# Performance work log

Measured on AMD Instinct MI355X. Metric: run time of the kernel, lower is better.

Reference implementation:

```python
import jax, jax.numpy as jnp
import numpy as np

B, N, K, D, L = 8, 1024, 16, 256, 3  # batch, max_node_num, neighbor fan-in, g_hidden_dim, layers


def setup_inputs() -> dict:
    key = jax.random.key(0)
    ks = jax.random.split(key, 14)
    f32 = jnp.float32
    scale = 1.0 / np.sqrt(D).astype(np.float32)
    randn = lambda k, s: jax.random.normal(k, s, dtype=f32)
    lens = jax.random.randint(ks[12], (B,), N // 2, N + 1)
    node_mask = (jnp.arange(N)[None, :] < lens[:, None]).astype(f32)
    return {
        "h0": randn(ks[0], (B, N, D)),
        "c0": randn(ks[1], (B, N, D)),
        "x_in": randn(ks[2], (B, N, D)),
        "x_out": randn(ks[3], (B, N, D)),
        "W_in": randn(ks[4], (4, D, D)) * scale,   # gates stacked: [i, o, f, cell]
        "U_in": randn(ks[5], (4, D, D)) * scale,
        "W_out": randn(ks[6], (4, D, D)) * scale,
        "U_out": randn(ks[7], (4, D, D)) * scale,
        "b": jnp.zeros((4, D), dtype=f32),
        "in_mask": jax.random.randint(ks[8], (B, N, K), 0, 2).astype(f32),
        "out_mask": jax.random.randint(ks[9], (B, N, K), 0, 2).astype(f32),
        "node_mask": node_mask,
        "in_nodes": jax.random.randint(ks[10], (B, N, K), 0, N, dtype=jnp.int32),
        "out_nodes": jax.random.randint(ks[11], (B, N, K), 0, N, dtype=jnp.int32),
        "num_layers": L,
    }


def _gather_agg(h, idx, nb_mask, node_mask):
    # h: [B,N,D], idx: [B,N,K] -> masked sum of neighbor hidden states [B,N,D]
    nb = jax.vmap(lambda hb, ib: hb[ib])(h, idx)           # [B,N,K,D]
    agg = jnp.einsum('bnkd,bnk->bnd', nb, nb_mask)
    return agg * node_mask[..., None]


def reference(h0, c0, x_in, x_out, W_in, U_in, W_out, U_out, b,
              in_mask, out_mask, node_mask, in_nodes, out_nodes, num_layers):
    h, c = h0, c0
    nm = node_mask[..., None]
    for _ in range(num_layers):
        h_in = _gather_agg(h, in_nodes, in_mask, node_mask)
        h_out = _gather_agg(h, out_nodes, out_mask, node_mask)
        # pre-activation for all 4 gates at once: [4,B,N,D]
        pre = (jnp.einsum('bnd,gde->gbne', x_in, W_in)
               + jnp.einsum('bnd,gde->gbne', h_in, U_in)
               + jnp.einsum('bnd,gde->gbne', x_out, W_out)
               + jnp.einsum('bnd,gde->gbne', h_out, U_out)
               + b[:, None, None, :])
        i_g = jax.nn.sigmoid(pre[0])
        o_g = jax.nn.sigmoid(pre[1])
        f_g = jax.nn.sigmoid(pre[2])
        g = jnp.tanh(pre[3])
        c = (f_g * c + i_g * g) * nm
        h = o_g * jnp.tanh(c) * nm
    return h
```

## Files before the change

### kernel.cpp

```cpp
#include <hip/hip_runtime.h>
#include <hip/hip_bf16.h>
#include <cstdint>
#include <cstddef>

typedef __hip_bfloat16 bf16;
typedef _Float16 f16;
typedef __attribute__((ext_vector_type(4))) float f32x4;
typedef __attribute__((ext_vector_type(8))) _Float16 f16x8;
typedef __attribute__((ext_vector_type(4))) _Float16 f16x4;
typedef __attribute__((ext_vector_type(4))) unsigned short u16x4;

#define BB 8
#define NN 1024
#define KK 16
#define DD 256
#define MM (BB * NN)
#define NLAYER 3

__device__ __forceinline__ float ldf(const void* p, size_t i, int isf32) {
  return isf32 ? ((const float*)p)[i] : __bfloat162float(((const bf16*)p)[i]);
}

__device__ __forceinline__ f32x4 ldf4(const void* p, size_t vi, int isf32) {
  f32x4 r;
  if (isf32) {
    r = ((const f32x4*)p)[vi];
  } else {
    u16x4 u = ((const u16x4*)p)[vi];
#pragma unroll
    for (int q = 0; q < 4; q++) {
      union { unsigned u; float f; } c;
      c.u = ((unsigned)u[q]) << 16;
      r[q] = c.f;
    }
  }
  return r;
}

__device__ __forceinline__ void gload_lds16(const void* g, void* l) {
  __builtin_amdgcn_global_load_lds(
      (const __attribute__((address_space(1))) unsigned int*)g,
      (__attribute__((address_space(3))) unsigned int*)l, 16, 0, 0);
}

__device__ __forceinline__ int detect_isf32_wave(const void* W) {
  int lane = threadIdx.x & 63;
  unsigned short b = ((const unsigned short*)W)[2 * lane];
  int e = (b >> 7) & 0xFF;
  int sane = ((e >= 105 && e <= 130) || (b & 0x7FFF) == 0) ? 1 : 0;
  unsigned long long m = __ballot(sane);
  return (__popcll(m) > 32) ? 0 : 1;
}

__device__ __forceinline__ float fsigmoid(float x) {
  float a = fminf(fmaxf(-1.44269504f * x, -126.f), 126.f);
  float e = __builtin_amdgcn_exp2f(a);
  return __builtin_amdgcn_rcpf(1.f + e);
}
__device__ __forceinline__ float ftanh(float x) {
  float a = fminf(fmaxf(2.88539008f * x, -126.f), 126.f);
  float e = __builtin_amdgcn_exp2f(a);
  return 1.f - 2.f * __builtin_amdgcn_rcpf(1.f + e);
}

struct Params {
  const void *h0, *c0, *x_in, *x_out, *W_in, *U_in, *W_out, *U_out, *bvec;
  const void *in_mask, *out_mask, *node_mask;
  const int *in_nodes, *out_nodes;
  float *biasI, *nmF, *inmF, *outmF, *XW;
  f16 *h_cur, *c_cur, *A_buf, *X_buf, *BT_W, *BT_U;
  void* outp;
};

#define PREP_VEC_TOTAL (256 + 2048 + 32768 + 32768 + 524288 + 524288)
#define PREP_BLOCKS (256 + (PREP_VEC_TOTAL + 255) / 256)
__global__ void prep_k(Params p) {
  __shared__ float tile[64][65];
  int isf32 = detect_isf32_wave(p.W_in);
  int b = blockIdx.x;
  int t = threadIdx.x;

  if (b < 256) {
    int bx = b & 3, by = (b >> 2) & 3, z = b >> 4;
    int g = z & 3, which = z >> 2;
    const void* src = (which == 0) ? p.W_in : (which == 1) ? p.W_out
                     : (which == 2) ? p.U_in : p.U_out;
    f16* dst = (which < 2) ? p.BT_W : p.BT_U;
    int colofs = (which & 1) * 256;
    size_t gbase = (size_t)g * DD * DD;
    int tx = t & 63, ty = t >> 6;
    int d0 = bx * 64, e0 = by * 64;
#pragma unroll
    for (int r = 0; r < 64; r += 4)
      tile[ty + r][tx] = ldf(src, gbase + (size_t)(d0 + ty + r) * DD + e0 + tx, isf32);
    __syncthreads();
#pragma unroll
    for (int r = 0; r < 64; r += 4)
      dst[(size_t)(4 * (e0 + ty + r) + g) * 512 + colofs + d0 + tx] = (f16)tile[tx][ty + r];
    return;
  }

  size_t i = (size_t)(b - 256) * 256 + t;
  const size_t V0 = 256;
  const size_t V1 = V0 + 2048;
  const size_t V2 = V1 + 32768;
  const size_t V3 = V2 + 32768;
  const size_t V4 = V3 + 524288;
  const size_t V5 = V4 + 524288;
  if (i < V0) {
    f32x4 r;
#pragma unroll
    for (int g = 0; g < 4; g++) r[g] = ldf(p.bvec, (size_t)g * 256 + i, isf32);
    ((f32x4*)p.biasI)[i] = r;
  } else if (i < V1) {
    ((f32x4*)p.nmF)[i - V0] = ldf4(p.node_mask, i - V0, isf32);
  } else if (i < V2) {
    ((f32x4*)p.inmF)[i - V1] = ldf4(p.in_mask, i - V1, isf32);
  } else if (i < V3) {
    ((f32x4*)p.outmF)[i - V2] = ldf4(p.out_mask, i - V2, isf32);
  } else if (i < V4) {
    size_t j = i - V3;
    f32x4 hv = ldf4(p.h0, j, isf32);
    f32x4 cv = ldf4(p.c0, j, isf32);
    f16x4 ho, co;
#pragma unroll
    for (int q = 0; q < 4; q++) { ho[q] = (f16)hv[q]; co[q] = (f16)cv[q]; }
    ((f16x4*)p.h_cur)[j] = ho;
    ((f16x4*)p.c_cur)[j] = co;
  } else if (i < V5) {
    size_t j = i - V4;
    size_t m = j >> 6, d4 = (j & 63) * 4;
    f32x4 xi = ldf4(p.x_in, j, isf32);
    f32x4 xo = ldf4(p.x_out, j, isf32);
    f16x4 a, bq;
#pragma unroll
    for (int q = 0; q < 4; q++) { a[q] = (f16)xi[q]; bq[q] = (f16)xo[q]; }
    *(f16x4*)(p.X_buf + m * 512 + d4)       = a;
    *(f16x4*)(p.X_buf + m * 512 + 256 + d4) = bq;
  }
}

__global__ void gather_k(Params p) {
  int wave = threadIdx.x >> 6;
  int lane = threadIdx.x & 63;
  int m = blockIdx.x * 4 + wave;
  int l5 = lane & 31, dir = lane >> 5;
  int myidx = 0; float mymask = 0.f;
  if (lane < 16)      { myidx = p.in_nodes[(size_t)m * KK + lane];
                        mymask = p.inmF[(size_t)m * KK + lane]; }
  else if (lane < 32) { myidx = p.out_nodes[(size_t)m * KK + lane - 16];
                        mymask = p.outmF[(size_t)m * KK + lane - 16]; }
  const f16* hb = p.h_cur + (size_t)(m >> 10) * NN * DD;
  float acc[8] = {};
#pragma unroll
  for (int k = 0; k < KK; k++) {
    int src = dir * 16 + k;
    int idxk = __shfl(myidx, src);
    float wk = __shfl(mymask, src);
    f16x8 v = *(const f16x8*)(hb + (size_t)idxk * DD + l5 * 8);
#pragma unroll
    for (int q = 0; q < 8; q++) acc[q] += wk * (float)v[q];
  }
  float nm = p.nmF[m];
  f16x8 o;
#pragma unroll
  for (int q = 0; q < 8; q++) o[q] = (f16)(acc[q] * nm);
  *(f16x8*)(p.A_buf + (size_t)m * 512 + dir * 256 + l5 * 8) = o;
}

__device__ __forceinline__ void gemm_core(const f16* gA, const f16* gB, char* smem,
                                          int t, int mBase, int nBase,
                                          f32x4 (&acc)[4][4]) {
  f16* As = (f16*)smem;
  f16* Bs = (f16*)(smem + 16384);
  int w = t >> 6, lane = t & 63;
  int wr = w >> 1, wc = w & 1;
  int row16 = lane & 15, kgrp = lane >> 4;
  int aoff[2][4], boff[2][4];
#pragma unroll
  for (int sub = 0; sub < 2; sub++) {
    int ch = ((sub * 4 + kgrp) ^ (row16 & 7)) * 8;
#pragma unroll
    for (int i = 0; i < 4; i++) aoff[sub][i] = (wr * 64 + 16 * i + row16) * 64 + ch;
#pragma unroll
    for (int j = 0; j < 4; j++) boff[sub][j] = (wc * 64 + 16 * j + row16) * 64 + ch;
  }
  int srow = t >> 3;
  int scol = ((t & 7) ^ (srow & 7)) * 8;
  const f16* ga0 = gA + (size_t)(mBase + srow) * 512 + scol;
  const f16* gb0 = gB + (size_t)(nBase + srow) * 512 + scol;
  for (int kt = 0; kt < 512; kt += 64) {
#pragma unroll
    for (int q = 0; q < 4; q++)
      gload_lds16(ga0 + kt + (size_t)(32 * q) * 512, As + q * 2048 + t * 8);
#pragma unroll
    for (int q = 0; q < 4; q++)
      gload_lds16(gb0 + kt + (size_t)(32 * q) * 512, Bs + q * 2048 + t * 8);
    __syncthreads();
#pragma unroll
    for (int sub = 0; sub < 2; sub++) {
      f16x8 af[4], bfr[4];
#pragma unroll
      for (int i = 0; i < 4; i++) af[i] = *(const f16x8*)(As + aoff[sub][i]);
#pragma unroll
      for (int j = 0; j < 4; j++) bfr[j] = *(const f16x8*)(Bs + boff[sub][j]);
#pragma unroll
      for (int i = 0; i < 4; i++)
#pragma unroll
        for (int j = 0; j < 4; j++)
          acc[i][j] = __builtin_amdgcn_mfma_f32_16x16x32_f16(af[i], bfr[j], acc[i][j], 0, 0, 0);
    }
    __syncthreads();
  }
}

__global__ __launch_bounds__(256, 3)
void gemmx_k(Params p) {
  __shared__ char smem[32768];
  int t = threadIdx.x;
  int w = t >> 6, lane = t & 63;
  int wc = w & 1, row16 = lane & 15;
  int mBase = blockIdx.x * 128, nBase = blockIdx.y * 128;
  f32x4 acc[4][4] = {};
  gemm_core(p.X_buf, p.BT_W, smem, t, mBase, nBase, acc);
  float bb[4];
#pragma unroll
  for (int j = 0; j < 4; j++) bb[j] = p.biasI[nBase + wc * 64 + 16 * j + row16];
  f32x4* dst = (f32x4*)p.XW + ((size_t)(blockIdx.y * 64 + blockIdx.x) * 256 + t) * 16;
#pragma unroll
  for (int i = 0; i < 4; i++)
#pragma unroll
    for (int j = 0; j < 4; j++) {
      f32x4 v = acc[i][j];
#pragma unroll
      for (int r = 0; r < 4; r++) v[r] += bb[j];
      dst[i * 4 + j] = v;
    }
}

__global__ __launch_bounds__(256, 3)
void gemm_k(Params p, int last) {
  __shared__ char smem[32768];
  float* tileF = (float*)smem;
  int isf32 = detect_isf32_wave(p.W_in);
  int t = threadIdx.x;
  int w = t >> 6, lane = t & 63;
  int wr = w >> 1, wc = w & 1;
  int row16 = lane & 15, kgrp = lane >> 4;
  int mBase = blockIdx.x * 128, nBase = blockIdx.y * 128;
  f32x4 acc[4][4];
  const f32x4* xw = (const f32x4*)p.XW + ((size_t)(blockIdx.y * 64 + blockIdx.x) * 256 + t) * 16;
#pragma unroll
  for (int i = 0; i < 4; i++)
#pragma unroll
    for (int j = 0; j < 4; j++) acc[i][j] = xw[i * 4 + j];
  gemm_core(p.A_buf, p.BT_U, smem, t, mBase, nBase, acc);

#pragma unroll
  for (int pp = 0; pp < 2; pp++) {
    __syncthreads();
    if (wc == pp) {
#pragma unroll
      for (int i = 0; i < 4; i++)
#pragma unroll
        for (int j = 0; j < 4; j++) {
          int cl = 16 * j + row16;
#pragma unroll
          for (int r = 0; r < 4; r++) {
            int rr = wr * 64 + 16 * i + 4 * kgrp + r;
            int ch = (cl >> 2) ^ (rr & 7);
            tileF[rr * 64 + ch * 4 + (cl & 3)] = acc[i][j][r];
          }
        }
    }
    __syncthreads();
    int el = t & 15;
    int nb = nBase + 64 * pp;
    int eb = nb >> 2;
#pragma unroll
    for (int rep = 0; rep < 8; rep++) {
      int ml = rep * 16 + (t >> 4);
      int gm = mBase + ml;
      f32x4 vals = *(const f32x4*)(tileF + ml * 64 + ((el ^ (ml & 7))) * 4);
      float nm = p.nmF[gm];
      size_t ci = (size_t)gm * DD + eb + el;
      float cold = (float)p.c_cur[ci];
      float ig = fsigmoid(vals[0]);
      float og = fsigmoid(vals[1]);
      float fg = fsigmoid(vals[2]);
      float gg = ftanh(vals[3]);
      float cn = (fg * cold + ig * gg) * nm;
      float hn = og * ftanh(cn) * nm;
      p.c_cur[ci] = (f16)cn;
      p.h_cur[ci] = (f16)hn;
      if (last) {
        if (isf32) ((float*)p.outp)[ci] = hn;
        else       ((bf16*)p.outp)[ci] = __float2bfloat16(hn);
      }
    }
  }
}

extern "C" void kernel_launch(void* const* d_in, const int* in_sizes, int n_in,
                              void* d_out, int out_size, void* d_ws, size_t ws_size,
                              hipStream_t stream) {
  char* ws = (char*)d_ws;
  f16*   h_cur = (f16*)(ws + 256);
  f16*   c_cur = h_cur + (size_t)MM * DD;
  f16*   A_buf = c_cur + (size_t)MM * DD;
  f16*   X_buf = A_buf + (size_t)MM * 512;
  f16*   BT_W  = X_buf + (size_t)MM * 512;
  f16*   BT_U  = BT_W + (size_t)1024 * 512;
  float* XW    = (float*)(BT_U + (size_t)1024 * 512);
  float* biasI = XW + (size_t)MM * 1024;
  float* nmF   = biasI + 1024;
  float* inmF  = nmF + MM;
  float* outmF = inmF + (size_t)MM * KK;

  Params p;
  p.h0 = d_in[0]; p.c0 = d_in[1]; p.x_in = d_in[2]; p.x_out = d_in[3];
  p.W_in = d_in[4]; p.U_in = d_in[5]; p.W_out = d_in[6]; p.U_out = d_in[7];
  p.bvec = d_in[8]; p.in_mask = d_in[9]; p.out_mask = d_in[10]; p.node_mask = d_in[11];
  p.in_nodes = (const int*)d_in[12]; p.out_nodes = (const int*)d_in[13];
  p.biasI = biasI; p.nmF = nmF; p.inmF = inmF; p.outmF = outmF; p.XW = XW;
  p.h_cur = h_cur; p.c_cur = c_cur; p.A_buf = A_buf; p.X_buf = X_buf;
  p.BT_W = BT_W; p.BT_U = BT_U;
  p.outp = d_out;

  prep_k<<<PREP_BLOCKS, 256, 0, stream>>>(p);
  gemmx_k<<<dim3(MM / 128, 8), 256, 0, stream>>>(p);
  for (int l = 0; l < NLAYER; l++) {
    gather_k<<<MM / 4, 256, 0, stream>>>(p);
    gemm_k<<<dim3(MM / 128, 8), 256, 0, stream>>>(p, l == NLAYER - 1);
  }
}
```

Baseline: 225.3 us.

## Fuse all phases into one persistent cooperative kernel with grid barriers

Replaces the eight separate launches (prep, input GEMM, and three gather/recurrent-GEMM pairs) with one persistent kernel of 512 blocks that runs each phase in turn, separated by a software grid barrier built on atomics. Gather work is redistributed so each block handles 16 nodes, and the first gather overlaps with the input GEMM inside the same barrier interval. The aim is to remove per-launch overhead and the tail gaps between kernels. In exchange it adds barrier spin costs, caps occupancy at 2 blocks per CU through the launch bound, and relies on all blocks being co-resident, with a non-cooperative fallback that could deadlock.

```diff
diff --git a/kernel.cpp b/kernel.cpp
--- a/kernel.cpp
+++ b/kernel.cpp
@@ -16,6 +16,8 @@
 #define DD 256
 #define MM (BB * NN)
 #define NLAYER 3
+#define NBLK 512
+#define NTHR 256
 
 __device__ __forceinline__ float ldf(const void* p, size_t i, int isf32) {
   return isf32 ? ((const float*)p)[i] : __bfloat162float(((const bf16*)p)[i]);
@@ -69,18 +71,33 @@
   const int *in_nodes, *out_nodes;
   float *biasI, *nmF, *inmF, *outmF, *XW;
   f16 *h_cur, *c_cur, *A_buf, *X_buf, *BT_W, *BT_U;
+  unsigned* bar;
   void* outp;
 };
 
+__device__ __forceinline__ void grid_sync(unsigned* bar) {
+  __syncthreads();
+  if (threadIdx.x == 0) {
+    __threadfence();
+    unsigned gen = atomicAdd(&bar[0], 0u);
+    if (atomicAdd(&bar[1], 1u) == (unsigned)gridDim.x - 1u) {
+      atomicExch(&bar[1], 0u);
+      atomicAdd(&bar[0], 1u);
+    } else {
+      while (atomicAdd(&bar[0], 0u) == gen) __builtin_amdgcn_s_sleep(2);
+    }
+    __threadfence();
+  }
+  __syncthreads();
+}
+
 #define PREP_VEC_TOTAL (256 + 2048 + 32768 + 32768 + 524288 + 524288)
-#define PREP_BLOCKS (256 + (PREP_VEC_TOTAL + 255) / 256)
-__global__ void prep_k(Params p) {
-  __shared__ float tile[64][65];
-  int isf32 = detect_isf32_wave(p.W_in);
+__device__ void prep_phase(const Params& p, char* smem, int isf32) {
   int b = blockIdx.x;
   int t = threadIdx.x;
 
   if (b < 256) {
+    float (*tile)[65] = (float(*)[65])smem;
     int bx = b & 3, by = (b >> 2) & 3, z = b >> 4;
     int g = z & 3, which = z >> 2;
     const void* src = (which == 0) ? p.W_in : (which == 1) ? p.W_out
@@ -97,75 +114,78 @@
 #pragma unroll
     for (int r = 0; r < 64; r += 4)
       dst[(size_t)(4 * (e0 + ty + r) + g) * 512 + colofs + d0 + tx] = (f16)tile[tx][ty + r];
-    return;
-  }
-
-  size_t i = (size_t)(b - 256) * 256 + t;
+  }
+
   const size_t V0 = 256;
   const size_t V1 = V0 + 2048;
   const size_t V2 = V1 + 32768;
   const size_t V3 = V2 + 32768;
   const size_t V4 = V3 + 524288;
   const size_t V5 = V4 + 524288;
-  if (i < V0) {
-    f32x4 r;
-#pragma unroll
-    for (int g = 0; g < 4; g++) r[g] = ldf(p.bvec, (size_t)g * 256 + i, isf32);
-    ((f32x4*)p.biasI)[i] = r;
-  } else if (i < V1) {
-    ((f32x4*)p.nmF)[i - V0] = ldf4(p.node_mask, i - V0, isf32);
-  } else if (i < V2) {
-    ((f32x4*)p.inmF)[i - V1] = ldf4(p.in_mask, i - V1, isf32);
-  } else if (i < V3) {
-    ((f32x4*)p.outmF)[i - V2] = ldf4(p.out_mask, i - V2, isf32);
-  } else if (i < V4) {
-    size_t j = i - V3;
-    f32x4 hv = ldf4(p.h0, j, isf32);
-    f32x4 cv = ldf4(p.c0, j, isf32);
-    f16x4 ho, co;
-#pragma unroll
-    for (int q = 0; q < 4; q++) { ho[q] = (f16)hv[q]; co[q] = (f16)cv[q]; }
-    ((f16x4*)p.h_cur)[j] = ho;
-    ((f16x4*)p.c_cur)[j] = co;
-  } else if (i < V5) {
-    size_t j = i - V4;
-    size_t m = j >> 6, d4 = (j & 63) * 4;
-    f32x4 xi = ldf4(p.x_in, j, isf32);
-    f32x4 xo = ldf4(p.x_out, j, isf32);
-    f16x4 a, bq;
-#pragma unroll
-    for (int q = 0; q < 4; q++) { a[q] = (f16)xi[q]; bq[q] = (f16)xo[q]; }
-    *(f16x4*)(p.X_buf + m * 512 + d4)       = a;
-    *(f16x4*)(p.X_buf + m * 512 + 256 + d4) = bq;
-  }
-}
-
-__global__ void gather_k(Params p) {
-  int wave = threadIdx.x >> 6;
-  int lane = threadIdx.x & 63;
-  int m = blockIdx.x * 4 + wave;
+  for (size_t i = (size_t)b * NTHR + t; i < V5; i += (size_t)NBLK * NTHR) {
+    if (i < V0) {
+      f32x4 r;
+#pragma unroll
+      for (int g = 0; g < 4; g++) r[g] = ldf(p.bvec, (size_t)g * 256 + i, isf32);
+      ((f32x4*)p.biasI)[i] = r;
+    } else if (i < V1) {
+      ((f32x4*)p.nmF)[i - V0] = ldf4(p.node_mask, i - V0, isf32);
+    } else if (i < V2) {
+      ((f32x4*)p.inmF)[i - V1] = ldf4(p.in_mask, i - V1, isf32);
+    } else if (i < V3) {
+      ((f32x4*)p.outmF)[i - V2] = ldf4(p.out_mask, i - V2, isf32);
+    } else if (i < V4) {
+      size_t j = i - V3;
+      f32x4 hv = ldf4(p.h0, j, isf32);
+      f32x4 cv = ldf4(p.c0, j, isf32);
+      f16x4 ho, co;
+#pragma unroll
+      for (int q = 0; q < 4; q++) { ho[q] = (f16)hv[q]; co[q] = (f16)cv[q]; }
+      ((f16x4*)p.h_cur)[j] = ho;
+      ((f16x4*)p.c_cur)[j] = co;
+    } else {
+      size_t j = i - V4;
+      size_t m = j >> 6, d4 = (j & 63) * 4;
+      f32x4 xi = ldf4(p.x_in, j, isf32);
+      f32x4 xo = ldf4(p.x_out, j, isf32);
+      f16x4 a, bq;
+#pragma unroll
+      for (int q = 0; q < 4; q++) { a[q] = (f16)xi[q]; bq[q] = (f16)xo[q]; }
+      *(f16x4*)(p.X_buf + m * 512 + d4)       = a;
+      *(f16x4*)(p.X_buf + m * 512 + 256 + d4) = bq;
+    }
+  }
+}
+
+__device__ void gather_phase(const Params& p) {
+  int gid = blockIdx.x, t = threadIdx.x;
+  int wave = t >> 6, lane = t & 63;
   int l5 = lane & 31, dir = lane >> 5;
-  int myidx = 0; float mymask = 0.f;
-  if (lane < 16)      { myidx = p.in_nodes[(size_t)m * KK + lane];
-                        mymask = p.inmF[(size_t)m * KK + lane]; }
-  else if (lane < 32) { myidx = p.out_nodes[(size_t)m * KK + lane - 16];
-                        mymask = p.outmF[(size_t)m * KK + lane - 16]; }
-  const f16* hb = p.h_cur + (size_t)(m >> 10) * NN * DD;
-  float acc[8] = {};
-#pragma unroll
-  for (int k = 0; k < KK; k++) {
-    int src = dir * 16 + k;
-    int idxk = __shfl(myidx, src);
-    float wk = __shfl(mymask, src);
-    f16x8 v = *(const f16x8*)(hb + (size_t)idxk * DD + l5 * 8);
-#pragma unroll
-    for (int q = 0; q < 8; q++) acc[q] += wk * (float)v[q];
-  }
-  float nm = p.nmF[m];
-  f16x8 o;
-#pragma unroll
-  for (int q = 0; q < 8; q++) o[q] = (f16)(acc[q] * nm);
-  *(f16x8*)(p.A_buf + (size_t)m * 512 + dir * 256 + l5 * 8) = o;
+#pragma unroll
+  for (int it = 0; it < 4; it++) {
+    int m = gid * 16 + it * 4 + wave;
+    int myidx = 0; float mymask = 0.f;
+    if (lane < 16)      { myidx = p.in_nodes[(size_t)m * KK + lane];
+                          mymask = p.inmF[(size_t)m * KK + lane]; }
+    else if (lane < 32) { myidx = p.out_nodes[(size_t)m * KK + lane - 16];
+                          mymask = p.outmF[(size_t)m * KK + lane - 16]; }
+    const f16* hb = p.h_cur + (size_t)(m >> 10) * NN * DD;
+    float acc[8] = {};
+#pragma unroll
+    for (int k = 0; k < KK; k++) {
+      int src = dir * 16 + k;
+      int idxk = __shfl(myidx, src);
+      float wk = __shfl(mymask, src);
+      f16x8 v = *(const f16x8*)(hb + (size_t)idxk * DD + l5 * 8);
+#pragma unroll
+      for (int q = 0; q < 8; q++) acc[q] += wk * (float)v[q];
+    }
+    float nm = p.nmF[m];
+    f16x8 o;
+#pragma unroll
+    for (int q = 0; q < 8; q++) o[q] = (f16)(acc[q] * nm);
+    *(f16x8*)(p.A_buf + (size_t)m * 512 + dir * 256 + l5 * 8) = o;
+  }
 }
 
 __device__ __forceinline__ void gemm_core(const f16* gA, const f16* gB, char* smem,
@@ -214,42 +234,38 @@
   }
 }
 
-__global__ __launch_bounds__(256, 3)
-void gemmx_k(Params p) {
-  __shared__ char smem[32768];
-  int t = threadIdx.x;
+__device__ void gemmx_phase(const Params& p, char* smem) {
+  int gid = blockIdx.x, t = threadIdx.x;
   int w = t >> 6, lane = t & 63;
   int wc = w & 1, row16 = lane & 15;
-  int mBase = blockIdx.x * 128, nBase = blockIdx.y * 128;
+  int mb = gid & 63, nb = gid >> 6;
   f32x4 acc[4][4] = {};
-  gemm_core(p.X_buf, p.BT_W, smem, t, mBase, nBase, acc);
-  float bb[4];
-#pragma unroll
-  for (int j = 0; j < 4; j++) bb[j] = p.biasI[nBase + wc * 64 + 16 * j + row16];
-  f32x4* dst = (f32x4*)p.XW + ((size_t)(blockIdx.y * 64 + blockIdx.x) * 256 + t) * 16;
+  gemm_core(p.X_buf, p.BT_W, smem, t, mb * 128, nb * 128, acc);
+  float bb4[4];
+#pragma unroll
+  for (int j = 0; j < 4; j++) bb4[j] = p.biasI[nb * 128 + wc * 64 + 16 * j + row16];
+  f32x4* dst = (f32x4*)p.XW + ((size_t)(nb * 64 + mb) * 256 + t) * 16;
 #pragma unroll
   for (int i = 0; i < 4; i++)
 #pragma unroll
     for (int j = 0; j < 4; j++) {
       f32x4 v = acc[i][j];
 #pragma unroll
-      for (int r = 0; r < 4; r++) v[r] += bb[j];
+      for (int r = 0; r < 4; r++) v[r] += bb4[j];
       dst[i * 4 + j] = v;
     }
 }
 
-__global__ __launch_bounds__(256, 3)
-void gemm_k(Params p, int last) {
-  __shared__ char smem[32768];
+__device__ void gemm_phase(const Params& p, char* smem, int last, int isf32) {
   float* tileF = (float*)smem;
-  int isf32 = detect_isf32_wave(p.W_in);
-  int t = threadIdx.x;
+  int gid = blockIdx.x, t = threadIdx.x;
   int w = t >> 6, lane = t & 63;
   int wr = w >> 1, wc = w & 1;
   int row16 = lane & 15, kgrp = lane >> 4;
-  int mBase = blockIdx.x * 128, nBase = blockIdx.y * 128;
+  int mb = gid & 63, nb = gid >> 6;
+  int mBase = mb * 128, nBase = nb * 128;
   f32x4 acc[4][4];
-  const f32x4* xw = (const f32x4*)p.XW + ((size_t)(blockIdx.y * 64 + blockIdx.x) * 256 + t) * 16;
+  const f32x4* xw = (const f32x4*)p.XW + ((size_t)(nb * 64 + mb) * 256 + t) * 16;
 #pragma unroll
   for (int i = 0; i < 4; i++)
 #pragma unroll
@@ -275,8 +291,8 @@
     }
     __syncthreads();
     int el = t & 15;
-    int nb = nBase + 64 * pp;
-    int eb = nb >> 2;
+    int nb2 = nBase + 64 * pp;
+    int eb = nb2 >> 2;
 #pragma unroll
     for (int rep = 0; rep < 8; rep++) {
       int ml = rep * 16 + (t >> 4);
@@ -301,6 +317,27 @@
   }
 }
 
+__global__ __launch_bounds__(NTHR, 2)
+void fused_k(Params p) {
+  __shared__ __attribute__((aligned(16))) char smem[32768];
+  int isf32 = detect_isf32_wave(p.W_in);
+
+  prep_phase(p, smem, isf32);
+  grid_sync(p.bar);
+  gather_phase(p);
+  gemmx_phase(p, smem);
+  grid_sync(p.bar);
+  gemm_phase(p, smem, 0, isf32);
+  grid_sync(p.bar);
+  gather_phase(p);
+  grid_sync(p.bar);
+  gemm_phase(p, smem, 0, isf32);
+  grid_sync(p.bar);
+  gather_phase(p);
+  grid_sync(p.bar);
+  gemm_phase(p, smem, 1, isf32);
+}
+
 extern "C" void kernel_launch(void* const* d_in, const int* in_sizes, int n_in,
                               void* d_out, int out_size, void* d_ws, size_t ws_size,
                               hipStream_t stream) {
@@ -325,12 +362,13 @@
   p.biasI = biasI; p.nmF = nmF; p.inmF = inmF; p.outmF = outmF; p.XW = XW;
   p.h_cur = h_cur; p.c_cur = c_cur; p.A_buf = A_buf; p.X_buf = X_buf;
   p.BT_W = BT_W; p.BT_U = BT_U;
+  p.bar = (unsigned*)ws;
   p.outp = d_out;
 
-  prep_k<<<PREP_BLOCKS, 256, 0, stream>>>(p);
-  gemmx_k<<<dim3(MM / 128, 8), 256, 0, stream>>>(p);
-  for (int l = 0; l < NLAYER; l++) {
-    gather_k<<<MM / 4, 256, 0, stream>>>(p);
-    gemm_k<<<dim3(MM / 128, 8), 256, 0, stream>>>(p, l == NLAYER - 1);
-  }
-}
+  hipMemsetAsync(ws, 0, 8, stream);
+  void* kargs[] = {(void*)&p};
+  if (hipLaunchCooperativeKernel((void*)fused_k, dim3(NBLK), dim3(NTHR),
+                                 kargs, 0, stream) != hipSuccess) {
+    fused_k<<<NBLK, NTHR, 0, stream>>>(p);
+  }
+}
```

New measurement: 598.2 us. +165.5%, slower.

## Double-buffer GEMM LDS tiles and store input projection XW in fp16

Applied to the files above, without the earlier changes.

Restructures the shared GEMM core loop to prefetch the next K-tile into a second LDS buffer while computing the current one, dropping one barrier per iteration. Separately, the precomputed input-projection plus bias buffer XW is stored as fp16 instead of fp32, halving its write and per-layer read traffic. LDS grows to 64 KB per block and launch bounds drop to 2 blocks per CU, trading occupancy for overlap. Storing XW in fp16 adds rounding error to the gate pre-activations.

```diff
diff --git a/kernel.cpp b/kernel.cpp
--- a/kernel.cpp
+++ b/kernel.cpp
@@ -67,8 +67,8 @@
   const void *h0, *c0, *x_in, *x_out, *W_in, *U_in, *W_out, *U_out, *bvec;
   const void *in_mask, *out_mask, *node_mask;
   const int *in_nodes, *out_nodes;
-  float *biasI, *nmF, *inmF, *outmF, *XW;
-  f16 *h_cur, *c_cur, *A_buf, *X_buf, *BT_W, *BT_U;
+  float *biasI, *nmF, *inmF, *outmF;
+  f16 *h_cur, *c_cur, *A_buf, *X_buf, *BT_W, *BT_U, *XW;
   void* outp;
 };
 
@@ -171,8 +171,6 @@
 __device__ __forceinline__ void gemm_core(const f16* gA, const f16* gB, char* smem,
                                           int t, int mBase, int nBase,
                                           f32x4 (&acc)[4][4]) {
-  f16* As = (f16*)smem;
-  f16* Bs = (f16*)(smem + 16384);
   int w = t >> 6, lane = t & 63;
   int wr = w >> 1, wc = w & 1;
   int row16 = lane & 15, kgrp = lane >> 4;
@@ -189,14 +187,35 @@
   int scol = ((t & 7) ^ (srow & 7)) * 8;
   const f16* ga0 = gA + (size_t)(mBase + srow) * 512 + scol;
   const f16* gb0 = gB + (size_t)(nBase + srow) * 512 + scol;
-  for (int kt = 0; kt < 512; kt += 64) {
+
+  {
+    f16* As = (f16*)smem;
+    f16* Bs = (f16*)(smem + 16384);
 #pragma unroll
     for (int q = 0; q < 4; q++)
-      gload_lds16(ga0 + kt + (size_t)(32 * q) * 512, As + q * 2048 + t * 8);
+      gload_lds16(ga0 + (size_t)(32 * q) * 512, As + q * 2048 + t * 8);
 #pragma unroll
     for (int q = 0; q < 4; q++)
-      gload_lds16(gb0 + kt + (size_t)(32 * q) * 512, Bs + q * 2048 + t * 8);
-    __syncthreads();
+      gload_lds16(gb0 + (size_t)(32 * q) * 512, Bs + q * 2048 + t * 8);
+  }
+  __syncthreads();
+
+#pragma unroll
+  for (int it = 0; it < 8; it++) {
+    int cur = it & 1;
+    if (it < 7) {
+      int kt = (it + 1) * 64;
+      f16* As = (f16*)(smem + (cur ^ 1) * 32768);
+      f16* Bs = (f16*)(smem + (cur ^ 1) * 32768 + 16384);
+#pragma unroll
+      for (int q = 0; q < 4; q++)
+        gload_lds16(ga0 + kt + (size_t)(32 * q) * 512, As + q * 2048 + t * 8);
+#pragma unroll
+      for (int q = 0; q < 4; q++)
+        gload_lds16(gb0 + kt + (size_t)(32 * q) * 512, Bs + q * 2048 + t * 8);
+    }
+    f16* As = (f16*)(smem + cur * 32768);
+    f16* Bs = (f16*)(smem + cur * 32768 + 16384);
 #pragma unroll
     for (int sub = 0; sub < 2; sub++) {
       f16x8 af[4], bfr[4];
@@ -214,33 +233,33 @@
   }
 }
 
-__global__ __launch_bounds__(256, 3)
+__global__ __launch_bounds__(256, 2)
 void gemmx_k(Params p) {
-  __shared__ char smem[32768];
+  __shared__ __attribute__((aligned(16))) char smem[65536];
   int t = threadIdx.x;
   int w = t >> 6, lane = t & 63;
   int wc = w & 1, row16 = lane & 15;
   int mBase = blockIdx.x * 128, nBase = blockIdx.y * 128;
   f32x4 acc[4][4] = {};
   gemm_core(p.X_buf, p.BT_W, smem, t, mBase, nBase, acc);
-  float bb[4];
-#pragma unroll
-  for (int j = 0; j < 4; j++) bb[j] = p.biasI[nBase + wc * 64 + 16 * j + row16];
-  f32x4* dst = (f32x4*)p.XW + ((size_t)(blockIdx.y * 64 + blockIdx.x) * 256 + t) * 16;
+  float bb4[4];
+#pragma unroll
+  for (int j = 0; j < 4; j++) bb4[j] = p.biasI[nBase + wc * 64 + 16 * j + row16];
+  f16x4* dst = (f16x4*)p.XW + ((size_t)(blockIdx.y * 64 + blockIdx.x) * 256 + t) * 16;
 #pragma unroll
   for (int i = 0; i < 4; i++)
 #pragma unroll
     for (int j = 0; j < 4; j++) {
-      f32x4 v = acc[i][j];
-#pragma unroll
-      for (int r = 0; r < 4; r++) v[r] += bb[j];
+      f16x4 v;
+#pragma unroll
+      for (int r = 0; r < 4; r++) v[r] = (f16)(acc[i][j][r] + bb4[j]);
       dst[i * 4 + j] = v;
     }
 }
 
-__global__ __launch_bounds__(256, 3)
+__global__ __launch_bounds__(256, 2)
 void gemm_k(Params p, int last) {
-  __shared__ char smem[32768];
+  __shared__ __attribute__((aligned(16))) char smem[65536];
   float* tileF = (float*)smem;
   int isf32 = detect_isf32_wave(p.W_in);
   int t = threadIdx.x;
@@ -249,11 +268,15 @@
   int row16 = lane & 15, kgrp = lane >> 4;
   int mBase = blockIdx.x * 128, nBase = blockIdx.y * 128;
   f32x4 acc[4][4];
-  const f32x4* xw = (const f32x4*)p.XW + ((size_t)(blockIdx.y * 64 + blockIdx.x) * 256 + t) * 16;
+  const f16x4* xw = (const f16x4*)p.XW + ((size_t)(blockIdx.y * 64 + blockIdx.x) * 256 + t) * 16;
 #pragma unroll
   for (int i = 0; i < 4; i++)
 #pragma unroll
-    for (int j = 0; j < 4; j++) acc[i][j] = xw[i * 4 + j];
+    for (int j = 0; j < 4; j++) {
+      f16x4 v = xw[i * 4 + j];
+#pragma unroll
+      for (int r = 0; r < 4; r++) acc[i][j][r] = (float)v[r];
+    }
   gemm_core(p.A_buf, p.BT_U, smem, t, mBase, nBase, acc);
 
 #pragma unroll
@@ -275,8 +298,8 @@
     }
     __syncthreads();
     int el = t & 15;
-    int nb = nBase + 64 * pp;
-    int eb = nb >> 2;
+    int nb2 = nBase + 64 * pp;
+    int eb = nb2 >> 2;
 #pragma unroll
     for (int rep = 0; rep < 8; rep++) {
       int ml = rep * 16 + (t >> 4);
@@ -311,8 +334,8 @@
   f16*   X_buf = A_buf + (size_t)MM * 512;
   f16*   BT_W  = X_buf + (size_t)MM * 512;
   f16*   BT_U  = BT_W + (size_t)1024 * 512;
-  float* XW    = (float*)(BT_U + (size_t)1024 * 512);
-  float* biasI = XW + (size_t)MM * 1024;
+  f16*   XW    = BT_U + (size_t)1024 * 512;
+  float* biasI = (float*)(XW + (size_t)MM * 1024);
   float* nmF   = biasI + 1024;
   float* inmF  = nmF + MM;
   float* outmF = inmF + (size_t)MM * KK;
@@ -322,9 +345,9 @@
   p.W_in = d_in[4]; p.U_in = d_in[5]; p.W_out = d_in[6]; p.U_out = d_in[7];
   p.bvec = d_in[8]; p.in_mask = d_in[9]; p.out_mask = d_in[10]; p.node_mask = d_in[11];
   p.in_nodes = (const int*)d_in[12]; p.out_nodes = (const int*)d_in[13];
-  p.biasI = biasI; p.nmF = nmF; p.inmF = inmF; p.outmF = outmF; p.XW = XW;
+  p.biasI = biasI; p.nmF = nmF; p.inmF = inmF; p.outmF = outmF;
   p.h_cur = h_cur; p.c_cur = c_cur; p.A_buf = A_buf; p.X_buf = X_buf;
-  p.BT_W = BT_W; p.BT_U = BT_U;
+  p.BT_W = BT_W; p.BT_U = BT_U; p.XW = XW;
   p.outp = d_out;
 
   prep_k<<<PREP_BLOCKS, 256, 0, stream>>>(p);
```

After: 218.4 us. -3.1%, faster.
